# Optimization experiments

Hardware: AMD Instinct MI355X
Metric: run time of the kernel (lower is better)

The kernel has to match this reference:

```python
import jax, jax.numpy as jnp
import numpy as np

N_NODES = 50000
N_EDGES = 800000
N_GRAPHS = 128


def gcn_conv(x, row, col, W, b, num_nodes):
    # GCNConv: x' = D^-1/2 (A + I) D^-1/2 (x W) + b, with self-loops added.
    h = x @ W  # [N, out]
    # append self-loops
    sl = jnp.arange(num_nodes, dtype=row.dtype)
    r = jnp.concatenate([row, sl])
    c = jnp.concatenate([col, sl])
    deg = jax.ops.segment_sum(jnp.ones_like(r, dtype=h.dtype), r, num_segments=num_nodes)
    dinv = jnp.where(deg > 0, jax.lax.rsqrt(deg), 0.0)
    norm = dinv[r] * dinv[c]  # [E+N]
    msg = h[c] * norm[:, None]  # gather + scale
    out = jax.ops.segment_sum(msg, r, num_segments=num_nodes)
    return out + b


def setup_inputs() -> dict:
    key = jax.random.key(0)
    k = jax.random.split(key, 6)
    x = jax.random.normal(k[0], (N_NODES, 256), dtype=jnp.float32)
    edge_index = jax.random.randint(k[1], (2, N_EDGES), 0, N_NODES, dtype=jnp.int32)
    batch = jnp.sort(jax.random.randint(k[2], (N_NODES,), 0, N_GRAPHS, dtype=jnp.int32))
    W1 = jax.random.normal(k[3], (256, 128), dtype=jnp.float32) * (1.0 / np.sqrt(256))
    b1 = jnp.zeros((128,), dtype=jnp.float32)
    W2 = jax.random.normal(k[4], (128, 32), dtype=jnp.float32) * (1.0 / np.sqrt(128))
    b2 = jnp.zeros((32,), dtype=jnp.float32)
    return {"x": x, "edge_index": edge_index, "batch": batch,
            "W1": W1, "b1": b1, "W2": W2, "b2": b2}


def reference(x, edge_index, batch, W1, b1, W2, b2):
    row, col = edge_index[0], edge_index[1]
    h = gcn_conv(x, row, col, W1, b1, N_NODES)
    h = jax.nn.relu(h)
    # dropout is identity in eval mode (training=False)
    h = gcn_conv(h, row, col, W2, b2, N_NODES)
    # global_mean_pool over batch ids
    sums = jax.ops.segment_sum(h, batch, num_segments=N_GRAPHS)
    cnts = jax.ops.segment_sum(jnp.ones((N_NODES,), dtype=h.dtype), batch, num_segments=N_GRAPHS)
    pooled = sums / jnp.clip(cnts, 1.0)[:, None]  # [G, num_classes]
    return jax.nn.log_softmax(pooled, axis=1)
```

## Files before the change

kernel.cpp:

```cpp
#include <hip/hip_runtime.h>
#include <hip/hip_bf16.h>
#include <math.h>

#define N_NODES 50000
#define N_EDGES 800000
#define N_GRAPHS 128
#define DIM0 256
#define DIM1 128
#define DIM2 32

#define NBUCK 196
#define NEB 98

using f32x4 = __attribute__((ext_vector_type(4))) float;
using s16x8 = __attribute__((ext_vector_type(8))) short;
typedef unsigned char u8;

__device__ inline unsigned bf16pack(float a, float b) {
    __hip_bfloat162 h2 = __float22bfloat162_rn(make_float2(a, b));
    unsigned r;
    __builtin_memcpy(&r, &h2, 4);
    return r;
}
__device__ inline float2 bf16x2(unsigned p) {
    return make_float2(__uint_as_float(p << 16), __uint_as_float(p & 0xffff0000u));
}

__device__ inline int featOf(int p) {
    return 32 * (p >> 5) + ((p >> 1) & 15) + 16 * (p & 1);
}

__global__ __launch_bounds__(256) void k_hist(const int* __restrict__ row, int* __restrict__ hist) {
    __shared__ int h[NBUCK];
    int b = blockIdx.x, t = threadIdx.x;
    if (t < NBUCK) h[t] = 0;
    __syncthreads();
#pragma unroll
    for (int i = 0; i < 8; ++i) {
        int idx = b * 2048 + i * 256 + t;
        if (idx < N_EDGES / 4) {
            int4 r4 = ((const int4*)row)[idx];
            atomicAdd(&h[r4.x >> 8], 1);
            atomicAdd(&h[r4.y >> 8], 1);
            atomicAdd(&h[r4.z >> 8], 1);
            atomicAdd(&h[r4.w >> 8], 1);
        }
    }
    __syncthreads();
    if (t < NBUCK) hist[b * NBUCK + t] = h[t];
}

__global__ __launch_bounds__(256) void k_place(const int* __restrict__ row, const int* __restrict__ col,
                                               const int* __restrict__ hist, uint* __restrict__ bb,
                                               int* __restrict__ bbase, int* __restrict__ btot,
                                               const float* __restrict__ W1, uint* __restrict__ W1b,
                                               const float* __restrict__ W2, uint* __restrict__ W2b,
                                               const int* __restrict__ batch, int* gstart,
                                               float* __restrict__ pooled) {
    __shared__ int cur[NBUCK];
    __shared__ int tot[NBUCK];
    __shared__ int sc[256];
    int blk = blockIdx.x, t = threadIdx.x;
    if (blk >= NEB) {
        if (blk == NEB + 16) {
            for (int i = t; i < N_GRAPHS * DIM2; i += 256) pooled[i] = 0.f;
            return;
        }
        int g = (blk - NEB) * 256 + t;
        {
            int s = g >> 9, tt = (g >> 6) & 7, q = (g >> 4) & 3, n = g & 15;
            int k0 = s * 32 + q * 8;
            int colw = tt * 16 + n;
            uint4 o;
            o.x = bf16pack(W1[(size_t)(k0 + 0) * DIM1 + colw], W1[(size_t)(k0 + 1) * DIM1 + colw]);
            o.y = bf16pack(W1[(size_t)(k0 + 2) * DIM1 + colw], W1[(size_t)(k0 + 3) * DIM1 + colw]);
            o.z = bf16pack(W1[(size_t)(k0 + 4) * DIM1 + colw], W1[(size_t)(k0 + 5) * DIM1 + colw]);
            o.w = bf16pack(W1[(size_t)(k0 + 6) * DIM1 + colw], W1[(size_t)(k0 + 7) * DIM1 + colw]);
            ((uint4*)W1b)[g] = o;
        }
        if (g < 512) {
            int s = g >> 7, tt = (g >> 6) & 1, l = g & 63;
            int n = tt * 16 + (l & 15);
            int kb = s * 32 + (l >> 4) * 8;
            uint4 o;
            o.x = bf16pack(W2[(size_t)featOf(kb + 0) * DIM2 + n], W2[(size_t)featOf(kb + 1) * DIM2 + n]);
            o.y = bf16pack(W2[(size_t)featOf(kb + 2) * DIM2 + n], W2[(size_t)featOf(kb + 3) * DIM2 + n]);
            o.z = bf16pack(W2[(size_t)featOf(kb + 4) * DIM2 + n], W2[(size_t)featOf(kb + 5) * DIM2 + n]);
            o.w = bf16pack(W2[(size_t)featOf(kb + 6) * DIM2 + n], W2[(size_t)featOf(kb + 7) * DIM2 + n]);
            ((uint4*)W2b)[g] = o;
        }
        if (g <= N_GRAPHS) {
            int lo = 0, hi = N_NODES;
            while (lo < hi) { int mid = (lo + hi) >> 1; if (batch[mid] < g) lo = mid + 1; else hi = mid; }
            gstart[g] = lo;
        }
        return;
    }
    int pre = 0, to = 0;
    for (int b2 = 0; b2 < NEB; ++b2) {
        int v = (t < NBUCK) ? hist[b2 * NBUCK + t] : 0;
        to += v;
        if (b2 < blk) pre += v;
    }
    if (t < NBUCK) tot[t] = to;
    sc[t] = (t < NBUCK) ? to : 0;
    __syncthreads();
    for (int off = 1; off < 256; off <<= 1) {
        int x = (t >= off) ? sc[t - off] : 0;
        __syncthreads();
        sc[t] += x;
        __syncthreads();
    }
    if (t < NBUCK) {
        int base = sc[t] - tot[t];
        cur[t] = base + pre;
        if (blk == 0) { bbase[t] = base; btot[t] = tot[t]; }
    }
    __syncthreads();
#pragma unroll
    for (int i = 0; i < 8; ++i) {
        int idx = blk * 2048 + i * 256 + t;
        if (idx < N_EDGES / 4) {
            int4 r4 = ((const int4*)row)[idx];
            int4 c4 = ((const int4*)col)[idx];
            int rs[4] = {r4.x, r4.y, r4.z, r4.w};
            int cs[4] = {c4.x, c4.y, c4.z, c4.w};
#pragma unroll
            for (int j = 0; j < 4; ++j) {
                int pos = atomicAdd(&cur[rs[j] >> 8], 1);
                bb[pos] = ((uint)(rs[j] & 255) << 16) | (uint)cs[j];
            }
        }
    }
}

__global__ __launch_bounds__(256) void k_build(const int* __restrict__ bbase, const int* __restrict__ btot,
                                               const uint* __restrict__ bb,
                                               int* __restrict__ offs, int* __restrict__ cnt,
                                               ushort* __restrict__ csr) {
    __shared__ int c256[256];
    __shared__ int cur256[256];
    __shared__ int wsum[4];
    int b = blockIdx.x, t = threadIdx.x;
    int start = bbase[b];
    int n = btot[b];
    c256[t] = 0;
    __syncthreads();
    for (int i = t; i < n; i += 256) atomicAdd(&c256[bb[start + i] >> 16], 1);
    __syncthreads();
    int w = t >> 6, l = t & 63;
    int v = c256[t];
    int incl = v;
#pragma unroll
    for (int off = 1; off < 64; off <<= 1) {
        int x = __shfl_up(incl, off, 64);
        if (l >= off) incl += x;
    }
    if (l == 63) wsum[w] = incl;
    __syncthreads();
    int woff = 0;
    for (int i = 0; i < w; ++i) woff += wsum[i];
    int excl = incl - v + woff;
    cur256[t] = excl;
    int r = b * 256 + t;
    if (r < N_NODES) { offs[r] = start + excl; cnt[r] = v; }
    __syncthreads();
    for (int i = t; i < n; i += 256) {
        uint e = bb[start + i];
        int pos = atomicAdd(&cur256[e >> 16], 1);
        csr[start + pos] = (ushort)(e & 0xFFFFu);
    }
}

#define G1_BM 128
#define AS_LD 20
__global__ __launch_bounds__(256) void k_gemm1(const float* __restrict__ X, const uint* __restrict__ W1b,
                                               const int* __restrict__ cnt,
                                               u8* __restrict__ q8, float* __restrict__ sArr) {
    __shared__ uint w1s[16384];
    __shared__ uint As[G1_BM * AS_LD];
    int t = threadIdx.x;
    int w = t >> 6, lane = t & 63, q = lane >> 4, m16 = lane & 15;
    int rowBase = blockIdx.x * G1_BM;

    {
        const uint4* src = (const uint4*)W1b;
        uint4* dst = (uint4*)w1s;
#pragma unroll
        for (int i = 0; i < 16; ++i) dst[i * 256 + t] = src[i * 256 + t];
    }

    f32x4 acc[2][8];
#pragma unroll
    for (int i = 0; i < 2; ++i)
#pragma unroll
        for (int j = 0; j < 8; ++j) acc[i][j] = (f32x4){0.f, 0.f, 0.f, 0.f};

    int ar = t >> 1, ah = t & 1;
    for (int s = 0; s < 8; ++s) {
        float4 f0 = {0,0,0,0}, f1 = {0,0,0,0}, f2 = {0,0,0,0}, f3 = {0,0,0,0};
        int grow = rowBase + ar;
        if (grow < N_NODES) {
            const float* src = X + (size_t)grow * DIM0 + s * 32 + ah * 16;
            f0 = *(const float4*)(src + 0);
            f1 = *(const float4*)(src + 4);
            f2 = *(const float4*)(src + 8);
            f3 = *(const float4*)(src + 12);
        }
        uint4 p0, p1;
        p0.x = bf16pack(f0.x, f0.y); p0.y = bf16pack(f0.z, f0.w);
        p0.z = bf16pack(f1.x, f1.y); p0.w = bf16pack(f1.z, f1.w);
        p1.x = bf16pack(f2.x, f2.y); p1.y = bf16pack(f2.z, f2.w);
        p1.z = bf16pack(f3.x, f3.y); p1.w = bf16pack(f3.z, f3.w);
        __syncthreads();
        *(uint4*)&As[ar * AS_LD + ah * 8 + 0] = p0;
        *(uint4*)&As[ar * AS_LD + ah * 8 + 4] = p1;
        __syncthreads();

        s16x8 af[2];
#pragma unroll
        for (int rt = 0; rt < 2; ++rt) {
            int arow = w * 32 + rt * 16 + m16;
            af[rt] = *(s16x8*)&As[arow * AS_LD + q * 4];
        }
#pragma unroll
        for (int tt = 0; tt < 8; ++tt) {
            s16x8 bf = *(s16x8*)&w1s[((s * 8 + tt) * 64 + lane) * 4];
            acc[0][tt] = __builtin_amdgcn_mfma_f32_16x16x32_bf16(af[0], bf, acc[0][tt], 0, 0, 0);
            acc[1][tt] = __builtin_amdgcn_mfma_f32_16x16x32_bf16(af[1], bf, acc[1][tt], 0, 0, 0);
        }
    }

#pragma unroll
    for (int rt = 0; rt < 2; ++rt) {
#pragma unroll
        for (int reg = 0; reg < 4; ++reg) {
            int row = rowBase + w * 32 + rt * 16 + q * 4 + reg;
            if (row < N_NODES) {
                float dv = rsqrtf((float)(cnt[row] + 1));
                float v[8];
#pragma unroll
                for (int u = 0; u < 4; ++u) {
                    v[2 * u]     = acc[rt][2 * u][reg] * dv;
                    v[2 * u + 1] = acc[rt][2 * u + 1][reg] * dv;
                }
                float m = 0.f;
#pragma unroll
                for (int u = 0; u < 8; ++u) m = fmaxf(m, fabsf(v[u]));
#pragma unroll
                for (int d = 1; d < 16; d <<= 1) m = fmaxf(m, __shfl_xor(m, d));
                float sinv = (m > 0.f) ? 127.0f / m : 0.f;
                float sc = m * (1.0f / 127.0f);
                u8* qr = q8 + (size_t)row * 128;
#pragma unroll
                for (int u = 0; u < 4; ++u) {
                    int q0 = (int)rintf(v[2 * u] * sinv) + 128;
                    int q1 = (int)rintf(v[2 * u + 1] * sinv) + 128;
                    ((ushort*)qr)[u * 16 + m16] = (ushort)(q0 | (q1 << 8));
                }
                if (m16 == 0) sArr[row] = sc;
            }
        }
    }
}

#define A1_LD 68
__global__ __launch_bounds__(512, 2) void k_agg1g2(const u8* __restrict__ q8, const float* __restrict__ sArr,
                                                   const int* __restrict__ cnt,
                                                   const int* __restrict__ offs, const ushort* __restrict__ csr,
                                                   const float* __restrict__ b1, const uint* __restrict__ W2b,
                                                   unsigned* __restrict__ h2u) {
    __shared__ uint a1tile[16 * A1_LD];
    __shared__ float sdi[16];
    int t = threadIdx.x;
    int wv = t >> 6, lane = t & 63;
    int grp = lane >> 4, li = lane & 15, sub = grp & 1;
    int nb16 = blockIdx.x * 16;
    int mA = wv * 2, mB = wv * 2 + 1;
    int nodeA = nb16 + mA, nodeB = nb16 + mB;
    int nA = cnt[nodeA], nB = cnt[nodeB];
    const ushort* cpA = csr + offs[nodeA];
    const ushort* cpB = csr + offs[nodeB];
    int ecA = (lane < nA) ? (int)cpA[lane] : 0;
    int ecB = (lane < nB) ? (int)cpB[lane] : 0;
    bool isA = grp < 2;
    int nSel = isA ? nA : nB;

    float acc[8];
#pragma unroll
    for (int u = 0; u < 8; ++u) acc[u] = 0.f;
    float ssum = 0.f;

    auto accum = [&](uint2 v, float s) {
        uint x = v.x, y = v.y;
        acc[0] += s * (float)(x & 255u);
        acc[1] += s * (float)((x >> 8) & 255u);
        acc[2] += s * (float)((x >> 16) & 255u);
        acc[3] += s * (float)(x >> 24);
        acc[4] += s * (float)(y & 255u);
        acc[5] += s * (float)((y >> 8) & 255u);
        acc[6] += s * (float)((y >> 16) & 255u);
        acc[7] += s * (float)(y >> 24);
    };
    auto fetch = [&](int k, uint2& v, float& s) {
        int item = 2 * k + sub;
        int cA_ = __shfl(ecA, item);
        int cB_ = __shfl(ecB, item);
        uint c = (uint)(isA ? cA_ : cB_);
        v = make_uint2(0u, 0u); s = 0.f;
        if (item < nSel) {
            v = *(const uint2*)(q8 + c * 128u + (uint)li * 8u);
            s = sArr[c];
        }
    };

    if (sub == 0) {
        uint selfNode = (uint)(isA ? nodeA : nodeB);
        uint2 sv = *(const uint2*)(q8 + selfNode * 128u + (uint)li * 8u);
        float ss = sArr[selfNode];
        accum(sv, ss);
        ssum += ss;
    }

    int KK = (max(nA, nB) + 1) >> 1;
    for (int k = 0; k < KK; k += 4) {
        uint2 v0, v1, v2, v3; float s0, s1, s2, s3;
        fetch(k, v0, s0);
        fetch(k + 1, v1, s1);
        fetch(k + 2, v2, s2);
        fetch(k + 3, v3, s3);
        accum(v0, s0); accum(v1, s1); accum(v2, s2); accum(v3, s3);
        ssum += (s0 + s1) + (s2 + s3);
    }

#pragma unroll
    for (int u = 0; u < 8; ++u) acc[u] += __shfl_xor(acc[u], 16);
    ssum += __shfl_xor(ssum, 16);
#pragma unroll
    for (int u = 0; u < 8; ++u) acc[u] -= 128.f * ssum;

    float diA = rsqrtf((float)(nA + 1));
    float diB = rsqrtf((float)(nB + 1));
    if (lane == 0) sdi[mA] = diA;
    if (lane == 32) sdi[mB] = diB;
    float di = isA ? diA : diB;
    int m = isA ? mA : mB;

    uint o0, o1, o2, o3;
    {
        int p = li * 4;
        int flo0 = 32 * (p >> 4) + (p & 15);
        float lo, hi;
        lo = fmaxf(acc[0] * di + b1[flo0 + 0], 0.f);  hi = fmaxf(acc[1] * di + b1[flo0 + 16], 0.f);
        o0 = bf16pack(lo, hi);
        lo = fmaxf(acc[2] * di + b1[flo0 + 1], 0.f);  hi = fmaxf(acc[3] * di + b1[flo0 + 17], 0.f);
        o1 = bf16pack(lo, hi);
        lo = fmaxf(acc[4] * di + b1[flo0 + 2], 0.f);  hi = fmaxf(acc[5] * di + b1[flo0 + 18], 0.f);
        o2 = bf16pack(lo, hi);
        lo = fmaxf(acc[6] * di + b1[flo0 + 3], 0.f);  hi = fmaxf(acc[7] * di + b1[flo0 + 19], 0.f);
        o3 = bf16pack(lo, hi);
    }
    if (sub == 0) {
        *(uint4*)&a1tile[m * A1_LD + li * 4] = make_uint4(o0, o1, o2, o3);
    }
    __syncthreads();

    if (wv == 0) {
        int q = lane >> 4, m16 = lane & 15;
        f32x4 accP = (f32x4){0.f, 0.f, 0.f, 0.f};
        f32x4 accQ = (f32x4){0.f, 0.f, 0.f, 0.f};
#pragma unroll
        for (int s = 0; s < 4; ++s) {
            s16x8 af = *(s16x8*)&a1tile[m16 * A1_LD + s * 16 + q * 4];
            s16x8 bf0 = *(const s16x8*)(W2b + (size_t)((s * 2 + 0) * 64 + lane) * 4);
            s16x8 bf1 = *(const s16x8*)(W2b + (size_t)((s * 2 + 1) * 64 + lane) * 4);
            accP = __builtin_amdgcn_mfma_f32_16x16x32_bf16(af, bf0, accP, 0, 0, 0);
            accQ = __builtin_amdgcn_mfma_f32_16x16x32_bf16(af, bf1, accQ, 0, 0, 0);
        }
#pragma unroll
        for (int r = 0; r < 4; ++r) {
            int node = nb16 + q * 4 + r;
            float dv = sdi[q * 4 + r];
            h2u[(size_t)node * 16 + m16] = bf16pack(accP[r] * dv, accQ[r] * dv);
        }
    }
}

__global__ __launch_bounds__(256) void k_agg2pool(const unsigned* __restrict__ h2u, const int* __restrict__ cnt,
                                                  const int* __restrict__ offs, const ushort* __restrict__ csr,
                                                  const int* __restrict__ batch, float* __restrict__ pooled) {
    __shared__ float2 red[16][16];
    int t = threadIdx.x;
    int nb16 = blockIdx.x * 16;
    int node = nb16 + (t >> 4);
    int l = t & 15;
    int sg = l >> 2, li = l & 3;
    int n = cnt[node];
    const ushort* cp = csr + offs[node];
    const char* hb = (const char*)h2u;

    float acc[8];
#pragma unroll
    for (int u = 0; u < 8; ++u) acc[u] = 0.f;

    auto accum = [&](uint4 v) {
        float2 a0 = bf16x2(v.x), a1 = bf16x2(v.y), a2 = bf16x2(v.z), a3 = bf16x2(v.w);
        acc[0] += a0.x; acc[1] += a0.y; acc[2] += a1.x; acc[3] += a1.y;
        acc[4] += a2.x; acc[5] += a2.y; acc[6] += a3.x; acc[7] += a3.y;
    };

    for (int base = 0; base < n; base += 16) {
        int m = min(16, n - base);
        int ec = (l < m) ? (int)cp[base + l] : 0;
        uint4 v0 = make_uint4(0u,0u,0u,0u), v1 = v0, v2 = v0, v3 = v0;
        int i0 = 0 + sg, i1 = 4 + sg, i2 = 8 + sg, i3 = 12 + sg;
        uint c0 = (uint)__shfl(ec, i0, 16);
        uint c1 = (uint)__shfl(ec, i1, 16);
        uint c2 = (uint)__shfl(ec, i2, 16);
        uint c3 = (uint)__shfl(ec, i3, 16);
        if (i0 < m) v0 = *(const uint4*)(hb + c0 * 64u + (uint)li * 16u);
        if (i1 < m) v1 = *(const uint4*)(hb + c1 * 64u + (uint)li * 16u);
        if (i2 < m) v2 = *(const uint4*)(hb + c2 * 64u + (uint)li * 16u);
        if (i3 < m) v3 = *(const uint4*)(hb + c3 * 64u + (uint)li * 16u);
        accum(v0); accum(v1); accum(v2); accum(v3);
    }

#pragma unroll
    for (int u = 0; u < 8; ++u) {
        acc[u] += __shfl_xor(acc[u], 4);
        acc[u] += __shfl_xor(acc[u], 8);
    }

    float di = rsqrtf((float)(n + 1));
    if (sg == 0) {
        uint4 sv = *(const uint4*)(hb + (uint)node * 64u + (uint)li * 16u);
        accum(sv);
        int mrow = t >> 4;
#pragma unroll
        for (int u = 0; u < 4; ++u)
            red[mrow][li * 4 + u] = make_float2(acc[2 * u] * di, acc[2 * u + 1] * di);
    }
    __syncthreads();
    if (t < 16) {
        float2 run = make_float2(0.f, 0.f);
        int gprev = batch[nb16];
        for (int m = 0; m < 16; ++m) {
            int g = batch[nb16 + m];
            if (g != gprev) {
                atomicAdd(&pooled[gprev * DIM2 + t], run.x);
                atomicAdd(&pooled[gprev * DIM2 + t + 16], run.y);
                run = make_float2(0.f, 0.f);
                gprev = g;
            }
            float2 v = red[m][t];
            run.x += v.x; run.y += v.y;
        }
        atomicAdd(&pooled[gprev * DIM2 + t], run.x);
        atomicAdd(&pooled[gprev * DIM2 + t + 16], run.y);
    }
}

__global__ __launch_bounds__(64) void k_final(const float* __restrict__ pooled, const int* __restrict__ gstart,
                                              const float* __restrict__ b2, float* __restrict__ out) {
    int g = blockIdx.x;
    int lane = threadIdx.x;
    float cntf = fmaxf((float)(gstart[g + 1] - gstart[g]), 1.0f);
    float val = 0.f, v = -INFINITY;
    if (lane < DIM2) {
        val = pooled[g * DIM2 + lane] / cntf + b2[lane];
        v = val;
    }
#pragma unroll
    for (int m = 16; m >= 1; m >>= 1) v = fmaxf(v, __shfl_xor(v, m, 32));
    float ex = (lane < DIM2) ? expf(val - v) : 0.f;
#pragma unroll
    for (int m = 16; m >= 1; m >>= 1) ex += __shfl_xor(ex, m, 32);
    if (lane < DIM2) out[g * DIM2 + lane] = val - v - logf(ex);
}

extern "C" void kernel_launch(void* const* d_in, const int* in_sizes, int n_in,
                              void* d_out, int out_size, void* d_ws, size_t ws_size,
                              hipStream_t stream) {
    const float* x     = (const float*)d_in[0];
    const int*   eidx  = (const int*)d_in[1];
    const int*   batch = (const int*)d_in[2];
    const float* W1    = (const float*)d_in[3];
    const float* b1    = (const float*)d_in[4];
    const float* W2    = (const float*)d_in[5];
    const float* b2    = (const float*)d_in[6];
    const int* row = eidx;
    const int* col = eidx + N_EDGES;
    float* out = (float*)d_out;

    char* p = (char*)d_ws;
    int*    cnt    = (int*)p;    p += (size_t)N_NODES * 4;
    int*    offs   = (int*)p;    p += (size_t)N_NODES * 4 + 16;
    int*    gstart = (int*)p;    p += 768;
    uint*   W1b    = (uint*)p;   p += 4096 * 16;
    uint*   W2b    = (uint*)p;   p += 512 * 16;
    int*    hist   = (int*)p;    p += (size_t)NEB * NBUCK * 4 + 32;
    int*    bbase  = (int*)p;    p += 1024;
    int*    btot   = (int*)p;    p += 1024;
    float*  pooled = (float*)p;  p += (size_t)N_GRAPHS * DIM2 * 4;
    uint*   bb     = (uint*)p;   p += (size_t)N_EDGES * 4;
    ushort* csr    = (ushort*)p; p += (size_t)N_EDGES * 2;
    u8*     q8     = (u8*)p;     p += (size_t)N_NODES * 128;
    float*  sArr   = (float*)p;  p += (size_t)N_NODES * 4;
    unsigned* h2u  = (unsigned*)p; p += (size_t)N_NODES * 16 * 4;

    k_hist<<<NEB, 256, 0, stream>>>(row, hist);
    k_place<<<NEB + 17, 256, 0, stream>>>(row, col, hist, bb, bbase, btot,
                                          W1, W1b, W2, W2b, batch, gstart, pooled);
    k_build<<<NBUCK, 256, 0, stream>>>(bbase, btot, bb, offs, cnt, csr);

    k_gemm1<<<(N_NODES + G1_BM - 1) / G1_BM, 256, 0, stream>>>(x, W1b, cnt, q8, sArr);
    k_agg1g2<<<N_NODES / 16, 512, 0, stream>>>(q8, sArr, cnt, offs, csr, b1, W2b, h2u);
    k_agg2pool<<<N_NODES / 16, 256, 0, stream>>>(h2u, cnt, offs, csr, batch, pooled);
    k_final<<<N_GRAPHS, 64, 0, stream>>>(pooled, gstart, b2, out);
}
```

Before: 180.7 us.

## Halve GEMM1 row tile and read W1 fragments from global instead of LDS

The first GEMM kernel now covers 64 rows per block instead of 128, with one 16-row MFMA tile per wave. It also drops the 64KB LDS staging of W1 and loads B fragments straight from global memory, relying on L1/L2 to cache them. This cuts LDS use so more blocks fit per CU and removes the per-block W1 copy, at the cost of repeated global/cache reads of W1 and less reuse of each B fragment across row tiles. The host launch grid must match the new tile size, and that code is not shown.

```diff
diff --git a/kernel.cpp b/kernel.cpp
--- a/kernel.cpp
+++ b/kernel.cpp
@@ -172,94 +172,70 @@
     }
 }
 
-#define G1_BM 128
+#define G1_BM 64
 #define AS_LD 20
 __global__ __launch_bounds__(256) void k_gemm1(const float* __restrict__ X, const uint* __restrict__ W1b,
                                                const int* __restrict__ cnt,
                                                u8* __restrict__ q8, float* __restrict__ sArr) {
-    __shared__ uint w1s[16384];
     __shared__ uint As[G1_BM * AS_LD];
     int t = threadIdx.x;
     int w = t >> 6, lane = t & 63, q = lane >> 4, m16 = lane & 15;
     int rowBase = blockIdx.x * G1_BM;
 
-    {
-        const uint4* src = (const uint4*)W1b;
-        uint4* dst = (uint4*)w1s;
-#pragma unroll
-        for (int i = 0; i < 16; ++i) dst[i * 256 + t] = src[i * 256 + t];
-    }
-
-    f32x4 acc[2][8];
-#pragma unroll
-    for (int i = 0; i < 2; ++i)
-#pragma unroll
-        for (int j = 0; j < 8; ++j) acc[i][j] = (f32x4){0.f, 0.f, 0.f, 0.f};
-
-    int ar = t >> 1, ah = t & 1;
+    f32x4 acc[8];
+#pragma unroll
+    for (int j = 0; j < 8; ++j) acc[j] = (f32x4){0.f, 0.f, 0.f, 0.f};
+
+    int ar = t >> 2, ac = t & 3;
     for (int s = 0; s < 8; ++s) {
-        float4 f0 = {0,0,0,0}, f1 = {0,0,0,0}, f2 = {0,0,0,0}, f3 = {0,0,0,0};
+        float4 f0 = {0,0,0,0}, f1 = {0,0,0,0};
         int grow = rowBase + ar;
         if (grow < N_NODES) {
-            const float* src = X + (size_t)grow * DIM0 + s * 32 + ah * 16;
+            const float* src = X + (size_t)grow * DIM0 + s * 32 + ac * 8;
             f0 = *(const float4*)(src + 0);
             f1 = *(const float4*)(src + 4);
-            f2 = *(const float4*)(src + 8);
-            f3 = *(const float4*)(src + 12);
-        }
-        uint4 p0, p1;
-        p0.x = bf16pack(f0.x, f0.y); p0.y = bf16pack(f0.z, f0.w);
-        p0.z = bf16pack(f1.x, f1.y); p0.w = bf16pack(f1.z, f1.w);
-        p1.x = bf16pack(f2.x, f2.y); p1.y = bf16pack(f2.z, f2.w);
-        p1.z = bf16pack(f3.x, f3.y); p1.w = bf16pack(f3.z, f3.w);
+        }
+        uint4 p;
+        p.x = bf16pack(f0.x, f0.y); p.y = bf16pack(f0.z, f0.w);
+        p.z = bf16pack(f1.x, f1.y); p.w = bf16pack(f1.z, f1.w);
         __syncthreads();
-        *(uint4*)&As[ar * AS_LD + ah * 8 + 0] = p0;
-        *(uint4*)&As[ar * AS_LD + ah * 8 + 4] = p1;
+        *(uint4*)&As[ar * AS_LD + ac * 4] = p;
         __syncthreads();
 
-        s16x8 af[2];
-#pragma unroll
-        for (int rt = 0; rt < 2; ++rt) {
-            int arow = w * 32 + rt * 16 + m16;
-            af[rt] = *(s16x8*)&As[arow * AS_LD + q * 4];
-        }
+        s16x8 af = *(s16x8*)&As[(w * 16 + m16) * AS_LD + q * 4];
 #pragma unroll
         for (int tt = 0; tt < 8; ++tt) {
-            s16x8 bf = *(s16x8*)&w1s[((s * 8 + tt) * 64 + lane) * 4];
-            acc[0][tt] = __builtin_amdgcn_mfma_f32_16x16x32_bf16(af[0], bf, acc[0][tt], 0, 0, 0);
-            acc[1][tt] = __builtin_amdgcn_mfma_f32_16x16x32_bf16(af[1], bf, acc[1][tt], 0, 0, 0);
-        }
-    }
-
-#pragma unroll
-    for (int rt = 0; rt < 2; ++rt) {
-#pragma unroll
-        for (int reg = 0; reg < 4; ++reg) {
-            int row = rowBase + w * 32 + rt * 16 + q * 4 + reg;
-            if (row < N_NODES) {
-                float dv = rsqrtf((float)(cnt[row] + 1));
-                float v[8];
-#pragma unroll
-                for (int u = 0; u < 4; ++u) {
-                    v[2 * u]     = acc[rt][2 * u][reg] * dv;
-                    v[2 * u + 1] = acc[rt][2 * u + 1][reg] * dv;
-                }
-                float m = 0.f;
-#pragma unroll
-                for (int u = 0; u < 8; ++u) m = fmaxf(m, fabsf(v[u]));
-#pragma unroll
-                for (int d = 1; d < 16; d <<= 1) m = fmaxf(m, __shfl_xor(m, d));
-                float sinv = (m > 0.f) ? 127.0f / m : 0.f;
-                float sc = m * (1.0f / 127.0f);
-                u8* qr = q8 + (size_t)row * 128;
-#pragma unroll
-                for (int u = 0; u < 4; ++u) {
-                    int q0 = (int)rintf(v[2 * u] * sinv) + 128;
-                    int q1 = (int)rintf(v[2 * u + 1] * sinv) + 128;
-                    ((ushort*)qr)[u * 16 + m16] = (ushort)(q0 | (q1 << 8));
-                }
-                if (m16 == 0) sArr[row] = sc;
+            s16x8 bf = *(const s16x8*)(W1b + (size_t)((s * 8 + tt) * 64 + lane) * 4);
+            acc[tt] = __builtin_amdgcn_mfma_f32_16x16x32_bf16(af, bf, acc[tt], 0, 0, 0);
+        }
+    }
+
+#pragma unroll
+    for (int reg = 0; reg < 4; ++reg) {
+        int row = rowBase + w * 16 + q * 4 + reg;
+        if (row < N_NODES) {
+            float dv = rsqrtf((float)(cnt[row] + 1));
+            float v[8];
+#pragma unroll
+            for (int u = 0; u < 4; ++u) {
+                v[2 * u]     = acc[2 * u][reg] * dv;
+                v[2 * u + 1] = acc[2 * u + 1][reg] * dv;
             }
+            float m = 0.f;
+#pragma unroll
+            for (int u = 0; u < 8; ++u) m = fmaxf(m, fabsf(v[u]));
+#pragma unroll
+            for (int d = 1; d < 16; d <<= 1) m = fmaxf(m, __shfl_xor(m, d));
+            float sinv = (m > 0.f) ? 127.0f / m : 0.f;
+            float sc = m * (1.0f / 127.0f);
+            u8* qr = q8 + (size_t)row * 128;
+#pragma unroll
+            for (int u = 0; u < 4; ++u) {
+                int q0 = (int)rintf(v[2 * u] * sinv) + 128;
+                int q1 = (int)rintf(v[2 * u + 1] * sinv) + 128;
+                ((ushort*)qr)[u * 16 + m16] = (ushort)(q0 | (q1 << 8));
+            }
+            if (m16 == 0) sArr[row] = sc;
         }
     }
 }
```

Result: no change. 183.0 us (+1.2%).
